# Kernel optimization log

Hardware: AMD Instinct MI355X
Metric: run time of the kernel (lower is better)

Reference implementation:

```python
import jax, jax.numpy as jnp
import numpy as np

N = 100000   # nodes
E = 3200000  # edges per graph
D = 16       # embedding_size, num_heads = 1
ATTN_SLOPE = 0.2   # DGL GATv2Conv negative_slope default
ACT_SLOPE = 0.01   # torch.nn.functional.leaky_relu default (activation arg)


def gatv2_layer(h, src, dst, W_src, b_src, W_dst, b_dst, attn):
    """DGL GATv2Conv with num_heads=1, activation=leaky_relu.
    h: [N, D]; src/dst: [E] int; W_*: [D, D]; b_*: [D]; attn: [D].
    """
    feat_src = h @ W_src + b_src          # [N, D]
    feat_dst = h @ W_dst + b_dst          # [N, D]
    el = feat_src[src]                    # [E, D] gather to edges
    e = jax.nn.leaky_relu(el + feat_dst[dst], ATTN_SLOPE)  # [E, D]
    score = e @ attn                      # [E] attention logits
    # segment softmax over incoming edges of each destination node
    smax = jax.ops.segment_max(score, dst, num_segments=N)
    smax = jnp.where(jnp.isfinite(smax), smax, 0.0)  # empty segments -> 0
    ex = jnp.exp(score - smax[dst])       # [E]
    denom = jax.ops.segment_sum(ex, dst, num_segments=N)  # [N]
    alpha = ex / denom[dst]               # [E]
    rst = jax.ops.segment_sum(alpha[:, None] * el, dst, num_segments=N)  # [N, D]
    return jax.nn.leaky_relu(rst, ACT_SLOPE)


def setup_inputs() -> dict:
    key = jax.random.key(0)
    ks = jax.random.split(key, 16)
    s = 1.0 / np.sqrt(D)
    return {
        "embedding": jax.random.normal(ks[0], (N, D), jnp.float32),
        "src1": jax.random.randint(ks[1], (E,), 0, N, jnp.int32),
        "dst1": jax.random.randint(ks[2], (E,), 0, N, jnp.int32),
        "src2": jax.random.randint(ks[3], (E,), 0, N, jnp.int32),
        "dst2": jax.random.randint(ks[4], (E,), 0, N, jnp.int32),
        "W_src1": jax.random.normal(ks[5], (D, D), jnp.float32) * s,
        "b_src1": jnp.zeros((D,), jnp.float32),
        "W_dst1": jax.random.normal(ks[6], (D, D), jnp.float32) * s,
        "b_dst1": jnp.zeros((D,), jnp.float32),
        "attn1": jax.random.normal(ks[7], (D,), jnp.float32) * s,
        "W_src2": jax.random.normal(ks[8], (D, D), jnp.float32) * s,
        "b_src2": jnp.zeros((D,), jnp.float32),
        "W_dst2": jax.random.normal(ks[9], (D, D), jnp.float32) * s,
        "b_dst2": jnp.zeros((D,), jnp.float32),
        "attn2": jax.random.normal(ks[10], (D,), jnp.float32) * s,
    }


def reference(embedding, src1, dst1, src2, dst2,
              W_src1, b_src1, W_dst1, b_dst1, attn1,
              W_src2, b_src2, W_dst2, b_dst2, attn2):
    user2item = gatv2_layer(embedding, src1, dst1, W_src1, b_src1, W_dst1, b_dst1, attn1)
    item_influence = gatv2_layer(user2item, src2, dst2, W_src2, b_src2, W_dst2, b_dst2, attn2)
    return item_influence  # [N, D]
```

## Files before the change

### kernel.cpp

```cpp
#include <hip/hip_runtime.h>
#include <hip/hip_fp16.h>

#define D 16
#define R 64
#define RBITS 6
#define RMASK 63
#define STRIDE 2560
#define CAP 2560
#define ACCT 512
#define KPT (CAP / ACCT)
#define EPB 8192
#define K1T 1024
#define NB2 1664
#define ATTN_SLOPE 0.2f
#define ACT_SLOPE 0.01f

__device__ __forceinline__ float leaky_a(float v) {
    return v > 0.f ? v : ATTN_SLOPE * v;
}
__device__ __forceinline__ float2 h2f(unsigned u) {
    __half2 h = *(__half2*)&u;
    return __half22float2(h);
}


__device__ void binscatter_tile(int tile, const int* __restrict__ src,
                                const int* __restrict__ dst,
                                int* __restrict__ gcur, unsigned* __restrict__ binned,
                                int E, int NB, char* sb) {
    unsigned* sorted = (unsigned*)sb;
    unsigned short* sposb = (unsigned short*)(sb + 32768);
    int* soffs = (int*)(sb + 49152);
    int* delta = (int*)(sb + 49152 + 4 * NB2);
    int* swsum = (int*)(sb + 49152 + 8 * NB2);
    int tid = threadIdx.x;
    int base = tile * EPB;
    int count = E - base;
    if (count > EPB) count = EPB;
    bool full = (count == EPB);

    for (int i = tid; i < NB; i += K1T) soffs[i] = 0;
    __syncthreads();
    int dd[8];
    if (full) {
        const int4* d4 = (const int4*)(dst + base);
        int4 a = d4[tid], b = d4[K1T + tid];
        dd[0] = a.x; dd[1] = a.y; dd[2] = a.z; dd[3] = a.w;
        dd[4] = b.x; dd[5] = b.y; dd[6] = b.z; dd[7] = b.w;
#pragma unroll
        for (int m = 0; m < 8; m++) atomicAdd(&soffs[dd[m] >> RBITS], 1);
    } else {
        for (int k = 0; k < 8; k++) {
            int e = base + k * K1T + tid;
            if (e < E) atomicAdd(&soffs[dst[e] >> RBITS], 1);
        }
    }
    __syncthreads();
    int i0 = 2 * tid, i1 = 2 * tid + 1;
    int a0 = (i0 < NB) ? soffs[i0] : 0;
    int a1 = (i1 < NB) ? soffs[i1] : 0;
    int pair = a0 + a1;
    int lane = tid & 63, w = tid >> 6;
    int x = pair;
#pragma unroll
    for (int ofs = 1; ofs < 64; ofs <<= 1) {
        int y = __shfl_up(x, ofs, 64);
        if (lane >= ofs) x += y;
    }
    if (lane == 63) swsum[w] = x;
    __syncthreads();
    if (w == 0) {
        int v = (lane < 16) ? swsum[lane] : 0;
        int s = v;
#pragma unroll
        for (int ofs = 1; ofs < 16; ofs <<= 1) {
            int y = __shfl_up(s, ofs, 64);
            if (lane >= ofs) s += y;
        }
        if (lane < 16) swsum[lane] = s - v;
    }
    __syncthreads();
    int excl = x - pair + swsum[w];
    __syncthreads();
    if (i0 < NB) {
        soffs[i0] = excl;
        if (a0 > 0) {
            int res = atomicAdd(&gcur[i0], a0);
            delta[i0] = i0 * STRIDE + res - excl;
        }
    }
    if (i1 < NB) {
        soffs[i1] = excl + a0;
        if (a1 > 0) {
            int res = atomicAdd(&gcur[i1], a1);
            delta[i1] = i1 * STRIDE + res - (excl + a0);
        }
    }
    __syncthreads();
    if (full) {
        const int4* s4 = (const int4*)(src + base);
        int4 sa = s4[tid], sb4 = s4[K1T + tid];
        int ss[8] = {sa.x, sa.y, sa.z, sa.w, sb4.x, sb4.y, sb4.z, sb4.w};
#pragma unroll
        for (int m = 0; m < 8; m++) {
            int b = dd[m] >> RBITS;
            int r = atomicAdd(&soffs[b], 1);
            sorted[r] = ((unsigned)ss[m] << RBITS) | (unsigned)(dd[m] & RMASK);
            sposb[r] = (unsigned short)b;
        }
    } else {
        for (int k = 0; k < 8; k++) {
            int e = base + k * K1T + tid;
            if (e < E) {
                int dv = dst[e];
                int b = dv >> RBITS;
                int r = atomicAdd(&soffs[b], 1);
                sorted[r] = ((unsigned)src[e] << RBITS) | (unsigned)(dv & RMASK);
                sposb[r] = (unsigned short)b;
            }
        }
    }
    __syncthreads();
#pragma unroll
    for (int m = 0; m < 8; m++) {
        int p = m * K1T + tid;
        if (p < count) {
            int b = sposb[p];
            int pos = p + delta[b];
            if (pos < (b + 1) * STRIDE) binned[pos] = sorted[p];
        }
    }
}

__device__ void transform_tile(int tile, const float* __restrict__ h,
                               const float* __restrict__ Ws, const float* __restrict__ bs,
                               const float* __restrict__ Wd, const float* __restrict__ bd,
                               __half* __restrict__ fsh, float* __restrict__ fdst,
                               int N, char* sb) {
    float* sWs = (float*)sb;
    float* sWd = sWs + 256;
    float* sbs = sWd + 256;
    float* sbd = sbs + 16;
    int t = threadIdx.x;
    if (t < 256) { sWs[t] = Ws[t]; sWd[t] = Wd[t]; }
    if (t < 16) { sbs[t] = bs[t]; sbd[t] = bd[t]; }
    __syncthreads();
    int n = tile * K1T + t;
    if (n >= N) return;
    float hv[D];
    const float4* h4 = (const float4*)(h + (size_t)n * D);
#pragma unroll
    for (int k = 0; k < 4; k++) {
        float4 v = h4[k];
        hv[4 * k] = v.x; hv[4 * k + 1] = v.y; hv[4 * k + 2] = v.z; hv[4 * k + 3] = v.w;
    }
    float os[D], od[D];
#pragma unroll
    for (int d = 0; d < D; d++) {
        float ss = sbs[d];
        float sd = sbd[d];
#pragma unroll
        for (int k = 0; k < D; k++) {
            ss += hv[k] * sWs[k * D + d];
            sd += hv[k] * sWd[k * D + d];
        }
        os[d] = ss; od[d] = sd;
    }
    unsigned us[8];
#pragma unroll
    for (int k = 0; k < 8; k++) {
        __half2 hh = __floats2half2_rn(os[2 * k], os[2 * k + 1]);
        us[k] = *(unsigned*)&hh;
    }
    uint4* fo = (uint4*)(fsh + (size_t)n * D);
    fo[0] = make_uint4(us[0], us[1], us[2], us[3]);
    fo[1] = make_uint4(us[4], us[5], us[6], us[7]);
    float4* fd4 = (float4*)(fdst + (size_t)n * D);
#pragma unroll
    for (int k = 0; k < 4; k++)
        fd4[k] = make_float4(od[4 * k], od[4 * k + 1], od[4 * k + 2], od[4 * k + 3]);
}

__global__ void __launch_bounds__(K1T)
k1_kernel(const float* h, const float* Ws, const float* bs,
          const float* Wd, const float* bd,
          __half* fsh, float* fdst,
          const int* srcA, const int* dstA, int* gA, unsigned* binnedA, int EA,
          const int* srcB, const int* dstB, int* gB, unsigned* binnedB, int EB,
          int N, int NB, int B1, int B2, int TT) {
    __shared__ __align__(16) char sb[49152 + 8 * NB2 + 64];
    int bid = blockIdx.x;
    if (bid < B1) {
        binscatter_tile(bid, srcA, dstA, gA, binnedA, EA, NB, sb);
    } else if (bid < B1 + B2) {
        binscatter_tile(bid - B1, srcB, dstB, gB, binnedB, EB, NB, sb);
    } else {
        int t = bid - B1 - B2;
        if (t < TT) transform_tile(t, h, Ws, bs, Wd, bd, fsh, fdst, N, sb);
    }
}


template <bool DO_TAIL>
__global__ void __launch_bounds__(ACCT)
acc_kernel(const unsigned* __restrict__ binned, const int* __restrict__ gcur,
           const __half* __restrict__ fsh, const float* __restrict__ fdst,
           const float* __restrict__ attn, float* __restrict__ out,
           __half* __restrict__ fs2h, float* __restrict__ fd2,
           const float* __restrict__ Ws2, const float* __restrict__ bs2,
           const float* __restrict__ Wd2, const float* __restrict__ bd2,
           int N) {
    __shared__ float sfd[R * D];
    __shared__ int ebuf[CAP];
    __shared__ float exbuf[CAP];
    __shared__ int cstart[R + 1];
    __shared__ int cur[R];
    __shared__ float wtail[544];
    int b = blockIdx.x;
    int tid = threadIdx.x;
    int node0 = b * R;
    int nn = N - node0;
    if (nn > R) nn = R;
    for (int i = tid; i < nn * D; i += ACCT) sfd[i] = fdst[node0 * D + i];
    if (tid <= R) cstart[tid] = 0;
    if (DO_TAIL) {
        if (tid < 256) { wtail[tid] = Ws2[tid]; wtail[256 + tid] = Wd2[tid]; }
        if (tid < 16) { wtail[512 + tid] = bs2[tid]; wtail[528 + tid] = bd2[tid]; }
    }

    float av[D];
#pragma unroll
    for (int k = 0; k < D; k++) av[k] = attn[k];

    int cnt = gcur[b];
    if (cnt > CAP) cnt = CAP;
    int base = b * STRIDE;

    unsigned pls[KPT];
#pragma unroll
    for (int k = 0; k < KPT; k++) {
        int j = k * ACCT + tid;
        pls[k] = (j < cnt) ? binned[base + j] : 0xFFFFFFFFu;
    }
    __syncthreads();

    const uint4* fsh4 = (const uint4*)fsh;
    const uint2* fsq = (const uint2*)fsh;
    const float4* sfd4 = (const float4*)sfd;

#pragma unroll
    for (int k = 0; k < KPT; k++)
        if (pls[k] != 0xFFFFFFFFu) atomicAdd(&cstart[pls[k] & RMASK], 1);

    float exs[KPT];
#pragma unroll
    for (int k = 0; k + 1 < KPT; k += 2) {
        unsigned q0 = pls[k], q1 = pls[k + 1];
        uint4 ua0, ub0, ua1, ub1;
        if (q0 != 0xFFFFFFFFu) {
            int s = q0 >> RBITS;
            ua0 = fsh4[2 * s]; ub0 = fsh4[2 * s + 1];
        }
        if (q1 != 0xFFFFFFFFu) {
            int s = q1 >> RBITS;
            ua1 = fsh4[2 * s]; ub1 = fsh4[2 * s + 1];
        }
        if (q0 != 0xFFFFFFFFu) {
            int loc = q0 & RMASK;
            float4 f0 = sfd4[loc * 4 + 0], f1 = sfd4[loc * 4 + 1];
            float4 f2 = sfd4[loc * 4 + 2], f3 = sfd4[loc * 4 + 3];
            float2 c0 = h2f(ua0.x), c1 = h2f(ua0.y), c2 = h2f(ua0.z), c3 = h2f(ua0.w);
            float2 c4 = h2f(ub0.x), c5 = h2f(ub0.y), c6 = h2f(ub0.z), c7 = h2f(ub0.w);
            float p = leaky_a(c0.x + f0.x) * av[0]  + leaky_a(c0.y + f0.y) * av[1]
                    + leaky_a(c1.x + f0.z) * av[2]  + leaky_a(c1.y + f0.w) * av[3]
                    + leaky_a(c2.x + f1.x) * av[4]  + leaky_a(c2.y + f1.y) * av[5]
                    + leaky_a(c3.x + f1.z) * av[6]  + leaky_a(c3.y + f1.w) * av[7]
                    + leaky_a(c4.x + f2.x) * av[8]  + leaky_a(c4.y + f2.y) * av[9]
                    + leaky_a(c5.x + f2.z) * av[10] + leaky_a(c5.y + f2.w) * av[11]
                    + leaky_a(c6.x + f3.x) * av[12] + leaky_a(c6.y + f3.y) * av[13]
                    + leaky_a(c7.x + f3.z) * av[14] + leaky_a(c7.y + f3.w) * av[15];
            exs[k] = __expf(p);
        }
        if (q1 != 0xFFFFFFFFu) {
            int loc = q1 & RMASK;
            float4 f0 = sfd4[loc * 4 + 0], f1 = sfd4[loc * 4 + 1];
            float4 f2 = sfd4[loc * 4 + 2], f3 = sfd4[loc * 4 + 3];
            float2 c0 = h2f(ua1.x), c1 = h2f(ua1.y), c2 = h2f(ua1.z), c3 = h2f(ua1.w);
            float2 c4 = h2f(ub1.x), c5 = h2f(ub1.y), c6 = h2f(ub1.z), c7 = h2f(ub1.w);
            float p = leaky_a(c0.x + f0.x) * av[0]  + leaky_a(c0.y + f0.y) * av[1]
                    + leaky_a(c1.x + f0.z) * av[2]  + leaky_a(c1.y + f0.w) * av[3]
                    + leaky_a(c2.x + f1.x) * av[4]  + leaky_a(c2.y + f1.y) * av[5]
                    + leaky_a(c3.x + f1.z) * av[6]  + leaky_a(c3.y + f1.w) * av[7]
                    + leaky_a(c4.x + f2.x) * av[8]  + leaky_a(c4.y + f2.y) * av[9]
                    + leaky_a(c5.x + f2.z) * av[10] + leaky_a(c5.y + f2.w) * av[11]
                    + leaky_a(c6.x + f3.x) * av[12] + leaky_a(c6.y + f3.y) * av[13]
                    + leaky_a(c7.x + f3.z) * av[14] + leaky_a(c7.y + f3.w) * av[15];
            exs[k + 1] = __expf(p);
        }
    }
    if (KPT & 1) {
        unsigned q0 = pls[KPT - 1];
        if (q0 != 0xFFFFFFFFu) {
            int s = q0 >> RBITS;
            uint4 ua0 = fsh4[2 * s], ub0 = fsh4[2 * s + 1];
            int loc = q0 & RMASK;
            float4 f0 = sfd4[loc * 4 + 0], f1 = sfd4[loc * 4 + 1];
            float4 f2 = sfd4[loc * 4 + 2], f3 = sfd4[loc * 4 + 3];
            float2 c0 = h2f(ua0.x), c1 = h2f(ua0.y), c2 = h2f(ua0.z), c3 = h2f(ua0.w);
            float2 c4 = h2f(ub0.x), c5 = h2f(ub0.y), c6 = h2f(ub0.z), c7 = h2f(ub0.w);
            float p = leaky_a(c0.x + f0.x) * av[0]  + leaky_a(c0.y + f0.y) * av[1]
                    + leaky_a(c1.x + f0.z) * av[2]  + leaky_a(c1.y + f0.w) * av[3]
                    + leaky_a(c2.x + f1.x) * av[4]  + leaky_a(c2.y + f1.y) * av[5]
                    + leaky_a(c3.x + f1.z) * av[6]  + leaky_a(c3.y + f1.w) * av[7]
                    + leaky_a(c4.x + f2.x) * av[8]  + leaky_a(c4.y + f2.y) * av[9]
                    + leaky_a(c5.x + f2.z) * av[10] + leaky_a(c5.y + f2.w) * av[11]
                    + leaky_a(c6.x + f3.x) * av[12] + leaky_a(c6.y + f3.y) * av[13]
                    + leaky_a(c7.x + f3.z) * av[14] + leaky_a(c7.y + f3.w) * av[15];
            exs[KPT - 1] = __expf(p);
        }
    }
    __syncthreads();
    if (tid < R) {
        int v = cstart[tid];
        int x = v;
#pragma unroll
        for (int ofs = 1; ofs < 64; ofs <<= 1) {
            int y = __shfl_up(x, ofs, 64);
            if (tid >= ofs) x += y;
        }
        cstart[tid] = x - v;
        cur[tid] = x - v;
        if (tid == R - 1) cstart[R] = x;
    }
    __syncthreads();
#pragma unroll
    for (int k = 0; k < KPT; k++) {
        unsigned pl = pls[k];
        if (pl != 0xFFFFFFFFu) {
            int r = atomicAdd(&cur[pl & RMASK], 1);
            ebuf[r] = (int)pl;
            exbuf[r] = exs[k];
        }
    }
    __syncthreads();

    int lane = tid & 63;
    int w = tid >> 6;
    int q = lane & 3;
    int s2 = (lane >> 2) & 3;
    int n2 = lane >> 4;

    float4 acc[2];
    float den[2];
#pragma unroll
    for (int i = 0; i < 2; i++) {
        acc[i] = make_float4(0.f, 0.f, 0.f, 0.f);
        den[i] = 0.f;
    }
#pragma unroll
    for (int i = 0; i < 2; i++) {
        int loc = w * 8 + i * 4 + n2;
        int kb = cstart[loc], ke = cstart[loc + 1];
        int k = kb + s2;
        for (; k + 12 < ke; k += 16) {
            int pl0 = ebuf[k];
            int pl1 = ebuf[k + 4];
            int pl2 = ebuf[k + 8];
            int pl3 = ebuf[k + 12];
            float ex0 = exbuf[k];
            float ex1 = exbuf[k + 4];
            float ex2 = exbuf[k + 8];
            float ex3 = exbuf[k + 12];
            uint2 u0 = fsq[(((unsigned)pl0) >> RBITS) * 4 + q];
            uint2 u1 = fsq[(((unsigned)pl1) >> RBITS) * 4 + q];
            uint2 u2 = fsq[(((unsigned)pl2) >> RBITS) * 4 + q];
            uint2 u3 = fsq[(((unsigned)pl3) >> RBITS) * 4 + q];
            float2 a01 = h2f(u0.x), a23 = h2f(u0.y);
            float2 b01 = h2f(u1.x), b23 = h2f(u1.y);
            float2 c01 = h2f(u2.x), c23 = h2f(u2.y);
            float2 d01 = h2f(u3.x), d23 = h2f(u3.y);
            acc[i].x += ex0 * a01.x + ex1 * b01.x + ex2 * c01.x + ex3 * d01.x;
            acc[i].y += ex0 * a01.y + ex1 * b01.y + ex2 * c01.y + ex3 * d01.y;
            acc[i].z += ex0 * a23.x + ex1 * b23.x + ex2 * c23.x + ex3 * d23.x;
            acc[i].w += ex0 * a23.y + ex1 * b23.y + ex2 * c23.y + ex3 * d23.y;
            den[i] += (ex0 + ex1) + (ex2 + ex3);
        }
        for (; k < ke; k += 4) {
            int pl = ebuf[k];
            float ex = exbuf[k];
            uint2 u = fsq[(((unsigned)pl) >> RBITS) * 4 + q];
            float2 a01 = h2f(u.x), a23 = h2f(u.y);
            acc[i].x += ex * a01.x;
            acc[i].y += ex * a01.y;
            acc[i].z += ex * a23.x;
            acc[i].w += ex * a23.y;
            den[i] += ex;
        }
    }
#pragma unroll
    for (int i = 0; i < 2; i++) {
        float4 a = acc[i];
        float dn = den[i];
#pragma unroll
        for (int m = 4; m <= 8; m <<= 1) {
            a.x += __shfl_xor(a.x, m, 16);
            a.y += __shfl_xor(a.y, m, 16);
            a.z += __shfl_xor(a.z, m, 16);
            a.w += __shfl_xor(a.w, m, 16);
            dn += __shfl_xor(dn, m, 16);
        }
        int loc = w * 8 + i * 4 + n2;
        if (s2 == 0 && loc < nn) {
            float inv = dn > 0.f ? 1.f / dn : 0.f;
            float4 v;
            v.x = a.x * inv; v.x = v.x > 0.f ? v.x : ACT_SLOPE * v.x;
            v.y = a.y * inv; v.y = v.y > 0.f ? v.y : ACT_SLOPE * v.y;
            v.z = a.z * inv; v.z = v.z > 0.f ? v.z : ACT_SLOPE * v.z;
            v.w = a.w * inv; v.w = v.w > 0.f ? v.w : ACT_SLOPE * v.w;
            if (DO_TAIL) {
                *(float4*)&sfd[loc * D + q * 4] = v;
            } else {
                ((float4*)out)[(size_t)(node0 + loc) * 4 + q] = v;
            }
        }
    }
    if (DO_TAIL) {
        __syncthreads();
        int loc = tid >> 2, qq = tid & 3;
        if (tid < 256 && loc < nn) {
            float hvv[16];
#pragma unroll
            for (int k = 0; k < 16; k++) hvv[k] = sfd[loc * D + k];
            float s0 = wtail[512 + 4 * qq], s1 = wtail[513 + 4 * qq];
            float s2v = wtail[514 + 4 * qq], s3 = wtail[515 + 4 * qq];
            float d0 = wtail[528 + 4 * qq], d1 = wtail[529 + 4 * qq];
            float d2v = wtail[530 + 4 * qq], d3 = wtail[531 + 4 * qq];
#pragma unroll
            for (int k = 0; k < 16; k++) {
                float hk = hvv[k];
                const float* wr = &wtail[k * 16 + 4 * qq];
                const float* wr2 = &wtail[256 + k * 16 + 4 * qq];
                s0 += hk * wr[0]; s1 += hk * wr[1]; s2v += hk * wr[2]; s3 += hk * wr[3];
                d0 += hk * wr2[0]; d1 += hk * wr2[1]; d2v += hk * wr2[2]; d3 += hk * wr2[3];
            }
            __half2 p0 = __floats2half2_rn(s0, s1), p1 = __floats2half2_rn(s2v, s3);
            *(uint2*)(fs2h + (size_t)(node0 + loc) * D + 4 * qq) =
                make_uint2(*(unsigned*)&p0, *(unsigned*)&p1);
            *(float4*)(fd2 + (size_t)(node0 + loc) * D + 4 * qq) =
                make_float4(d0, d1, d2v, d3);
        }
    }
}


extern "C" void kernel_launch(void* const* d_in, const int* in_sizes, int n_in,
                              void* d_out, int out_size, void* d_ws, size_t ws_size,
                              hipStream_t stream) {
    const float* emb = (const float*)d_in[0];
    const int* src1 = (const int*)d_in[1];
    const int* dst1 = (const int*)d_in[2];
    const int* src2 = (const int*)d_in[3];
    const int* dst2 = (const int*)d_in[4];
    const float* Wsrc1 = (const float*)d_in[5];
    const float* bsrc1 = (const float*)d_in[6];
    const float* Wdst1 = (const float*)d_in[7];
    const float* bdst1 = (const float*)d_in[8];
    const float* attn1 = (const float*)d_in[9];
    const float* Wsrc2 = (const float*)d_in[10];
    const float* bsrc2 = (const float*)d_in[11];
    const float* Wdst2 = (const float*)d_in[12];
    const float* bdst2 = (const float*)d_in[13];
    const float* attn2 = (const float*)d_in[14];

    const int N = in_sizes[0] / D;
    const int E1 = in_sizes[1];
    const int E2 = in_sizes[3];
    const int NB = (N + R - 1) / R;
    const size_t ndf = (size_t)N * D;

    float* ws = (float*)d_ws;
    float* fd1 = ws;
    float* fd2 = fd1 + ndf;
    __half* fs1h = (__half*)(fd2 + ndf);
    __half* fs2h = fs1h + ndf;
    int* gA = (int*)(fs2h + ndf);
    int* gB = gA + NB2;
    unsigned* binned1 = (unsigned*)(gB + NB2);
    unsigned* binned2big = binned1 + (size_t)NB * STRIDE;
    size_t bigNeed = (size_t)((char*)(binned2big + (size_t)NB * STRIDE) - (char*)d_ws);
    bool big = ws_size >= bigNeed;
    (void)n_in; (void)out_size;

    const int B1 = (E1 + EPB - 1) / EPB;
    const int B2 = (E2 + EPB - 1) / EPB;
    const int TT = (N + K1T - 1) / K1T;

    (void)hipMemsetAsync(gA, 0, 2 * NB2 * sizeof(int), stream);

    if (big) {
        k1_kernel<<<B1 + B2 + TT, K1T, 0, stream>>>(
            emb, Wsrc1, bsrc1, Wdst1, bdst1, fs1h, fd1,
            src1, dst1, gA, binned1, E1,
            src2, dst2, gB, binned2big, E2,
            N, NB, B1, B2, TT);
        acc_kernel<true><<<NB, ACCT, 0, stream>>>(
            binned1, gA, fs1h, fd1, attn1, nullptr,
            fs2h, fd2, Wsrc2, bsrc2, Wdst2, bdst2, N);
        acc_kernel<false><<<NB, ACCT, 0, stream>>>(
            binned2big, gB, fs2h, fd2, attn2, (float*)d_out,
            nullptr, nullptr, nullptr, nullptr, nullptr, nullptr, N);
    } else {
        k1_kernel<<<B1 + TT, K1T, 0, stream>>>(
            emb, Wsrc1, bsrc1, Wdst1, bdst1, fs1h, fd1,
            src1, dst1, gA, binned1, E1,
            src2, dst2, gB, binned1, 0,
            N, NB, B1, 0, TT);
        acc_kernel<true><<<NB, ACCT, 0, stream>>>(
            binned1, gA, fs1h, fd1, attn1, nullptr,
            fs2h, fd2, Wsrc2, bsrc2, Wdst2, bdst2, N);
        k1_kernel<<<B2, K1T, 0, stream>>>(
            emb, Wsrc1, bsrc1, Wdst1, bdst1, fs1h, fd1,
            src2, dst2, gB, binned1, E2,
            src2, dst2, gB, binned1, 0,
            N, NB, B2, 0, 0);
        acc_kernel<false><<<NB, ACCT, 0, stream>>>(
            binned1, gB, fs2h, fd2, attn2, (float*)d_out,
            nullptr, nullptr, nullptr, nullptr, nullptr, nullptr, N);
    }
}
```

Measured before the change: 234.2 us.

## Halve binscatter tile size and pack bin indices to raise k1 occupancy

Halves the edges per block and threads per block in the binning kernel and shrinks the shared-memory scratch to match. This allows more blocks per CU, and launch bounds now request 8. The src loads are hoisted ahead of the histogram and packed into key values early. Bucket indices are packed two per register to cut register pressure. The prefix scan now handles four bins per thread, and one redundant barrier is removed. The trade-offs are twice as many tiles, which means more global atomics on gcur, and less work per block.

```diff
diff --git a/kernel.cpp b/kernel.cpp
--- a/kernel.cpp
+++ b/kernel.cpp
@@ -9,8 +9,8 @@
 #define CAP 2560
 #define ACCT 512
 #define KPT (CAP / ACCT)
-#define EPB 8192
-#define K1T 1024
+#define EPB 4096
+#define K1T 512
 #define NB2 1664
 #define ATTN_SLOPE 0.2f
 #define ACT_SLOPE 0.01f
@@ -29,10 +29,10 @@
                                 int* __restrict__ gcur, unsigned* __restrict__ binned,
                                 int E, int NB, char* sb) {
     unsigned* sorted = (unsigned*)sb;
-    unsigned short* sposb = (unsigned short*)(sb + 32768);
-    int* soffs = (int*)(sb + 49152);
-    int* delta = (int*)(sb + 49152 + 4 * NB2);
-    int* swsum = (int*)(sb + 49152 + 8 * NB2);
+    unsigned short* sposb = (unsigned short*)(sb + 16384);
+    int* soffs = (int*)(sb + 24576);
+    int* delta = (int*)(sb + 24576 + 4 * NB2);
+    int* swsum = (int*)(sb + 24576 + 8 * NB2);
     int tid = threadIdx.x;
     int base = tile * EPB;
     int count = E - base;
@@ -41,14 +41,28 @@
 
     for (int i = tid; i < NB; i += K1T) soffs[i] = 0;
     __syncthreads();
-    int dd[8];
+
+    unsigned val[8];
+    unsigned bp[4];
     if (full) {
         const int4* d4 = (const int4*)(dst + base);
+        const int4* s4 = (const int4*)(src + base);
         int4 a = d4[tid], b = d4[K1T + tid];
-        dd[0] = a.x; dd[1] = a.y; dd[2] = a.z; dd[3] = a.w;
-        dd[4] = b.x; dd[5] = b.y; dd[6] = b.z; dd[7] = b.w;
-#pragma unroll
-        for (int m = 0; m < 8; m++) atomicAdd(&soffs[dd[m] >> RBITS], 1);
+        int4 sa = s4[tid], sb4 = s4[K1T + tid];
+        int dd[8] = {a.x, a.y, a.z, a.w, b.x, b.y, b.z, b.w};
+        int ss[8] = {sa.x, sa.y, sa.z, sa.w, sb4.x, sb4.y, sb4.z, sb4.w};
+#pragma unroll
+        for (int m = 0; m < 8; m++)
+            val[m] = ((unsigned)ss[m] << RBITS) | ((unsigned)dd[m] & RMASK);
+#pragma unroll
+        for (int m = 0; m < 4; m++)
+            bp[m] = ((unsigned)dd[2 * m] >> RBITS) |
+                    (((unsigned)dd[2 * m + 1] >> RBITS) << 16);
+#pragma unroll
+        for (int m = 0; m < 4; m++) {
+            atomicAdd(&soffs[bp[m] & 0xFFFFu], 1);
+            atomicAdd(&soffs[bp[m] >> 16], 1);
+        }
     } else {
         for (int k = 0; k < 8; k++) {
             int e = base + k * K1T + tid;
@@ -56,12 +70,14 @@
         }
     }
     __syncthreads();
-    int i0 = 2 * tid, i1 = 2 * tid + 1;
+    int i0 = 4 * tid;
     int a0 = (i0 < NB) ? soffs[i0] : 0;
-    int a1 = (i1 < NB) ? soffs[i1] : 0;
-    int pair = a0 + a1;
+    int a1 = (i0 + 1 < NB) ? soffs[i0 + 1] : 0;
+    int a2 = (i0 + 2 < NB) ? soffs[i0 + 2] : 0;
+    int a3 = (i0 + 3 < NB) ? soffs[i0 + 3] : 0;
+    int quad = a0 + a1 + a2 + a3;
     int lane = tid & 63, w = tid >> 6;
-    int x = pair;
+    int x = quad;
 #pragma unroll
     for (int ofs = 1; ofs < 64; ofs <<= 1) {
         int y = __shfl_up(x, ofs, 64);
@@ -70,43 +86,46 @@
     if (lane == 63) swsum[w] = x;
     __syncthreads();
     if (w == 0) {
-        int v = (lane < 16) ? swsum[lane] : 0;
+        int v = (lane < 8) ? swsum[lane] : 0;
         int s = v;
 #pragma unroll
-        for (int ofs = 1; ofs < 16; ofs <<= 1) {
+        for (int ofs = 1; ofs < 8; ofs <<= 1) {
             int y = __shfl_up(s, ofs, 64);
             if (lane >= ofs) s += y;
         }
-        if (lane < 16) swsum[lane] = s - v;
-    }
-    __syncthreads();
-    int excl = x - pair + swsum[w];
-    __syncthreads();
+        if (lane < 8) swsum[lane] = s - v;
+    }
+    __syncthreads();
+    int excl = x - quad + swsum[w];
+    int e0 = excl, e1 = excl + a0, e2 = e1 + a1, e3 = e2 + a2;
     if (i0 < NB) {
-        soffs[i0] = excl;
-        if (a0 > 0) {
-            int res = atomicAdd(&gcur[i0], a0);
-            delta[i0] = i0 * STRIDE + res - excl;
-        }
-    }
-    if (i1 < NB) {
-        soffs[i1] = excl + a0;
-        if (a1 > 0) {
-            int res = atomicAdd(&gcur[i1], a1);
-            delta[i1] = i1 * STRIDE + res - (excl + a0);
-        }
+        soffs[i0] = e0;
+        if (a0 > 0) { int res = atomicAdd(&gcur[i0], a0); delta[i0] = i0 * STRIDE + res - e0; }
+    }
+    if (i0 + 1 < NB) {
+        soffs[i0 + 1] = e1;
+        if (a1 > 0) { int res = atomicAdd(&gcur[i0 + 1], a1); delta[i0 + 1] = (i0 + 1) * STRIDE + res - e1; }
+    }
+    if (i0 + 2 < NB) {
+        soffs[i0 + 2] = e2;
+        if (a2 > 0) { int res = atomicAdd(&gcur[i0 + 2], a2); delta[i0 + 2] = (i0 + 2) * STRIDE + res - e2; }
+    }
+    if (i0 + 3 < NB) {
+        soffs[i0 + 3] = e3;
+        if (a3 > 0) { int res = atomicAdd(&gcur[i0 + 3], a3); delta[i0 + 3] = (i0 + 3) * STRIDE + res - e3; }
     }
     __syncthreads();
     if (full) {
-        const int4* s4 = (const int4*)(src + base);
-        int4 sa = s4[tid], sb4 = s4[K1T + tid];
-        int ss[8] = {sa.x, sa.y, sa.z, sa.w, sb4.x, sb4.y, sb4.z, sb4.w};
-#pragma unroll
-        for (int m = 0; m < 8; m++) {
-            int b = dd[m] >> RBITS;
-            int r = atomicAdd(&soffs[b], 1);
-            sorted[r] = ((unsigned)ss[m] << RBITS) | (unsigned)(dd[m] & RMASK);
-            sposb[r] = (unsigned short)b;
+#pragma unroll
+        for (int m = 0; m < 4; m++) {
+            int b0 = bp[m] & 0xFFFFu;
+            int r0 = atomicAdd(&soffs[b0], 1);
+            sorted[r0] = val[2 * m];
+            sposb[r0] = (unsigned short)b0;
+            int b1 = bp[m] >> 16;
+            int r1 = atomicAdd(&soffs[b1], 1);
+            sorted[r1] = val[2 * m + 1];
+            sposb[r1] = (unsigned short)b1;
         }
     } else {
         for (int k = 0; k < 8; k++) {
@@ -181,14 +200,14 @@
         fd4[k] = make_float4(od[4 * k], od[4 * k + 1], od[4 * k + 2], od[4 * k + 3]);
 }
 
-__global__ void __launch_bounds__(K1T)
+__global__ void __launch_bounds__(K1T, 8)
 k1_kernel(const float* h, const float* Ws, const float* bs,
           const float* Wd, const float* bd,
           __half* fsh, float* fdst,
           const int* srcA, const int* dstA, int* gA, unsigned* binnedA, int EA,
           const int* srcB, const int* dstB, int* gB, unsigned* binnedB, int EB,
           int N, int NB, int B1, int B2, int TT) {
-    __shared__ __align__(16) char sb[49152 + 8 * NB2 + 64];
+    __shared__ __align__(16) char sb[24576 + 8 * NB2 + 64];
     int bid = blockIdx.x;
     if (bid < B1) {
         binscatter_tile(bid, srcA, dstA, gA, binnedA, EA, NB, sb);
```

After: 312.8 us. 33.6% more time.

## Double edges per binning tile and reserve global bin slots once per tile

Applied to the files above, without the earlier changes.

Each binning tile now covers 16384 edges, handled as two 8192-edge chunks inside the block. A first histogram pass over the whole tile reserves global bin space with one atomic per bin, and each chunk then writes at running per-bin cursors. This halves the number of global atomics on gcur and the tile count, and makes each bin's writes longer and more contiguous. The cost is reading dst an extra time, more barriers, and half as many blocks to spread across the GPU.

```diff
diff --git a/kernel.cpp b/kernel.cpp
--- a/kernel.cpp
+++ b/kernel.cpp
@@ -9,7 +9,8 @@
 #define CAP 2560
 #define ACCT 512
 #define KPT (CAP / ACCT)
-#define EPB 8192
+#define EPB 16384
+#define CHK 8192
 #define K1T 1024
 #define NB2 1664
 #define ATTN_SLOPE 0.2f
@@ -31,103 +32,152 @@
     unsigned* sorted = (unsigned*)sb;
     unsigned short* sposb = (unsigned short*)(sb + 32768);
     int* soffs = (int*)(sb + 49152);
-    int* delta = (int*)(sb + 49152 + 4 * NB2);
+    int* wcur = (int*)(sb + 49152 + 4 * NB2);
     int* swsum = (int*)(sb + 49152 + 8 * NB2);
     int tid = threadIdx.x;
+    int lane = tid & 63, w = tid >> 6;
     int base = tile * EPB;
     int count = E - base;
     if (count > EPB) count = EPB;
-    bool full = (count == EPB);
-
-    for (int i = tid; i < NB; i += K1T) soffs[i] = 0;
-    __syncthreads();
-    int dd[8];
-    if (full) {
+
+    for (int i = tid; i < NB; i += K1T) wcur[i] = 0;
+    __syncthreads();
+
+    if (count == EPB) {
         const int4* d4 = (const int4*)(dst + base);
-        int4 a = d4[tid], b = d4[K1T + tid];
-        dd[0] = a.x; dd[1] = a.y; dd[2] = a.z; dd[3] = a.w;
-        dd[4] = b.x; dd[5] = b.y; dd[6] = b.z; dd[7] = b.w;
-#pragma unroll
-        for (int m = 0; m < 8; m++) atomicAdd(&soffs[dd[m] >> RBITS], 1);
+#pragma unroll
+        for (int m = 0; m < 4; m++) {
+            int4 a = d4[m * K1T + tid];
+            atomicAdd(&wcur[a.x >> RBITS], 1);
+            atomicAdd(&wcur[a.y >> RBITS], 1);
+            atomicAdd(&wcur[a.z >> RBITS], 1);
+            atomicAdd(&wcur[a.w >> RBITS], 1);
+        }
     } else {
-        for (int k = 0; k < 8; k++) {
+        for (int k = 0; k < 16; k++) {
             int e = base + k * K1T + tid;
-            if (e < E) atomicAdd(&soffs[dst[e] >> RBITS], 1);
-        }
-    }
-    __syncthreads();
+            if (e < E) atomicAdd(&wcur[dst[e] >> RBITS], 1);
+        }
+    }
+    __syncthreads();
+
+    for (int i = tid; i < NB; i += K1T) {
+        int c = wcur[i];
+        if (c > 0) {
+            int res = atomicAdd(&gcur[i], c);
+            wcur[i] = i * STRIDE + res;
+        }
+    }
+    __syncthreads();
+
     int i0 = 2 * tid, i1 = 2 * tid + 1;
-    int a0 = (i0 < NB) ? soffs[i0] : 0;
-    int a1 = (i1 < NB) ? soffs[i1] : 0;
-    int pair = a0 + a1;
-    int lane = tid & 63, w = tid >> 6;
-    int x = pair;
-#pragma unroll
-    for (int ofs = 1; ofs < 64; ofs <<= 1) {
-        int y = __shfl_up(x, ofs, 64);
-        if (lane >= ofs) x += y;
-    }
-    if (lane == 63) swsum[w] = x;
-    __syncthreads();
-    if (w == 0) {
-        int v = (lane < 16) ? swsum[lane] : 0;
-        int s = v;
-#pragma unroll
-        for (int ofs = 1; ofs < 16; ofs <<= 1) {
-            int y = __shfl_up(s, ofs, 64);
-            if (lane >= ofs) s += y;
-        }
-        if (lane < 16) swsum[lane] = s - v;
-    }
-    __syncthreads();
-    int excl = x - pair + swsum[w];
-    __syncthreads();
-    if (i0 < NB) {
-        soffs[i0] = excl;
-        if (a0 > 0) {
-            int res = atomicAdd(&gcur[i0], a0);
-            delta[i0] = i0 * STRIDE + res - excl;
-        }
-    }
-    if (i1 < NB) {
-        soffs[i1] = excl + a0;
-        if (a1 > 0) {
-            int res = atomicAdd(&gcur[i1], a1);
-            delta[i1] = i1 * STRIDE + res - (excl + a0);
-        }
-    }
-    __syncthreads();
-    if (full) {
-        const int4* s4 = (const int4*)(src + base);
-        int4 sa = s4[tid], sb4 = s4[K1T + tid];
-        int ss[8] = {sa.x, sa.y, sa.z, sa.w, sb4.x, sb4.y, sb4.z, sb4.w};
+    for (int c = 0; c < 2; c++) {
+        int cbase = base + c * CHK;
+        int cc = count - c * CHK;
+        if (cc <= 0) break;
+        if (cc > CHK) cc = CHK;
+        bool full = (cc == CHK);
+
+        for (int i = tid; i < NB; i += K1T) soffs[i] = 0;
+        __syncthreads();
+
+        if (full) {
+            const int4* d4 = (const int4*)(dst + cbase);
+            int4 a = d4[tid], b4 = d4[K1T + tid];
+            atomicAdd(&soffs[a.x >> RBITS], 1);
+            atomicAdd(&soffs[a.y >> RBITS], 1);
+            atomicAdd(&soffs[a.z >> RBITS], 1);
+            atomicAdd(&soffs[a.w >> RBITS], 1);
+            atomicAdd(&soffs[b4.x >> RBITS], 1);
+            atomicAdd(&soffs[b4.y >> RBITS], 1);
+            atomicAdd(&soffs[b4.z >> RBITS], 1);
+            atomicAdd(&soffs[b4.w >> RBITS], 1);
+        } else {
+            for (int k = 0; k < 8; k++) {
+                int e = cbase + k * K1T + tid;
+                if (e < E) atomicAdd(&soffs[dst[e] >> RBITS], 1);
+            }
+        }
+        __syncthreads();
+
+        int a0 = (i0 < NB) ? soffs[i0] : 0;
+        int a1 = (i1 < NB) ? soffs[i1] : 0;
+        int pair = a0 + a1;
+        int x = pair;
+#pragma unroll
+        for (int ofs = 1; ofs < 64; ofs <<= 1) {
+            int y = __shfl_up(x, ofs, 64);
+            if (lane >= ofs) x += y;
+        }
+        if (lane == 63) swsum[w] = x;
+        __syncthreads();
+        if (w == 0) {
+            int v = (lane < 16) ? swsum[lane] : 0;
+            int s = v;
+#pragma unroll
+            for (int ofs = 1; ofs < 16; ofs <<= 1) {
+                int y = __shfl_up(s, ofs, 64);
+                if (lane >= ofs) s += y;
+            }
+            if (lane < 16) swsum[lane] = s - v;
+        }
+        __syncthreads();
+        int excl = x - pair + swsum[w];
+        int e0 = excl, e1 = excl + a0;
+        int d0v = 0, d1v = 0;
+        if (i0 < NB) {
+            soffs[i0] = e0;
+            if (a0 > 0) { d0v = wcur[i0] - e0; wcur[i0] = d0v; }
+        }
+        if (i1 < NB) {
+            soffs[i1] = e1;
+            if (a1 > 0) { d1v = wcur[i1] - e1; wcur[i1] = d1v; }
+        }
+        __syncthreads();
+
+        if (full) {
+            const int4* d4 = (const int4*)(dst + cbase);
+            const int4* s4 = (const int4*)(src + cbase);
+            int4 a = d4[tid], b4 = d4[K1T + tid];
+            int4 sa = s4[tid], sb4 = s4[K1T + tid];
+            int dd[8] = {a.x, a.y, a.z, a.w, b4.x, b4.y, b4.z, b4.w};
+            int ss[8] = {sa.x, sa.y, sa.z, sa.w, sb4.x, sb4.y, sb4.z, sb4.w};
+#pragma unroll
+            for (int m = 0; m < 8; m++) {
+                int bb = dd[m] >> RBITS;
+                int r = atomicAdd(&soffs[bb], 1);
+                sorted[r] = ((unsigned)ss[m] << RBITS) | (unsigned)(dd[m] & RMASK);
+                sposb[r] = (unsigned short)bb;
+            }
+        } else {
+            for (int k = 0; k < 8; k++) {
+                int e = cbase + k * K1T + tid;
+                if (e < E) {
+                    int dv = dst[e];
+                    int bb = dv >> RBITS;
+                    int r = atomicAdd(&soffs[bb], 1);
+                    sorted[r] = ((unsigned)src[e] << RBITS) | (unsigned)(dv & RMASK);
+                    sposb[r] = (unsigned short)bb;
+                }
+            }
+        }
+        __syncthreads();
+
 #pragma unroll
         for (int m = 0; m < 8; m++) {
-            int b = dd[m] >> RBITS;
-            int r = atomicAdd(&soffs[b], 1);
-            sorted[r] = ((unsigned)ss[m] << RBITS) | (unsigned)(dd[m] & RMASK);
-            sposb[r] = (unsigned short)b;
-        }
-    } else {
-        for (int k = 0; k < 8; k++) {
-            int e = base + k * K1T + tid;
-            if (e < E) {
-                int dv = dst[e];
-                int b = dv >> RBITS;
-                int r = atomicAdd(&soffs[b], 1);
-                sorted[r] = ((unsigned)src[e] << RBITS) | (unsigned)(dv & RMASK);
-                sposb[r] = (unsigned short)b;
-            }
-        }
-    }
-    __syncthreads();
-#pragma unroll
-    for (int m = 0; m < 8; m++) {
-        int p = m * K1T + tid;
-        if (p < count) {
-            int b = sposb[p];
-            int pos = p + delta[b];
-            if (pos < (b + 1) * STRIDE) binned[pos] = sorted[p];
+            int p = m * K1T + tid;
+            if (p < cc) {
+                int bb = sposb[p];
+                int pos = p + wcur[bb];
+                if (pos < (bb + 1) * STRIDE) binned[pos] = sorted[p];
+            }
+        }
+        __syncthreads();
+
+        if (c == 0) {
+            if (i0 < NB && a0 > 0) wcur[i0] = d0v + e0 + a0;
+            if (i1 < NB && a1 > 0) wcur[i1] = d1v + e1 + a1;
+            __syncthreads();
         }
     }
 }
```

Result: no change. 235.2 us (+0.5%).

## Scatter edges directly to global bins, dropping the shared-memory local sort

Applied to the files above, without the earlier changes.

The binning pass no longer sorts each tile into shared memory with a prefix scan and then copies out. It now counts edges per bin, reserves a global range for each bin with one atomic, and has each thread write its edge straight to the global bin position using shared atomic cursors. The edges per block double while threads per block halve, the transform tile covers 1024 nodes with a loop, and the much smaller shared footprint plus launch bounds of 8 allow higher occupancy. The cost is that global writes are less coalesced, since consecutive threads write to scattered bins instead of sorted runs.

```diff
diff --git a/kernel.cpp b/kernel.cpp
--- a/kernel.cpp
+++ b/kernel.cpp
@@ -9,8 +9,9 @@
 #define CAP 2560
 #define ACCT 512
 #define KPT (CAP / ACCT)
-#define EPB 8192
-#define K1T 1024
+#define EPB 16384
+#define K1T 512
+#define TNODES 1024
 #define NB2 1664
 #define ATTN_SLOPE 0.2f
 #define ACT_SLOPE 0.01f
@@ -28,106 +29,77 @@
                                 const int* __restrict__ dst,
                                 int* __restrict__ gcur, unsigned* __restrict__ binned,
                                 int E, int NB, char* sb) {
-    unsigned* sorted = (unsigned*)sb;
-    unsigned short* sposb = (unsigned short*)(sb + 32768);
-    int* soffs = (int*)(sb + 49152);
-    int* delta = (int*)(sb + 49152 + 4 * NB2);
-    int* swsum = (int*)(sb + 49152 + 8 * NB2);
+    int* wcur = (int*)sb;
     int tid = threadIdx.x;
     int base = tile * EPB;
     int count = E - base;
     if (count > EPB) count = EPB;
-    bool full = (count == EPB);
-
-    for (int i = tid; i < NB; i += K1T) soffs[i] = 0;
-    __syncthreads();
-    int dd[8];
-    if (full) {
+    bool fullT = (count == EPB);
+
+    for (int i = tid; i < NB; i += K1T) wcur[i] = 0;
+    __syncthreads();
+
+    if (fullT) {
         const int4* d4 = (const int4*)(dst + base);
-        int4 a = d4[tid], b = d4[K1T + tid];
-        dd[0] = a.x; dd[1] = a.y; dd[2] = a.z; dd[3] = a.w;
-        dd[4] = b.x; dd[5] = b.y; dd[6] = b.z; dd[7] = b.w;
-#pragma unroll
-        for (int m = 0; m < 8; m++) atomicAdd(&soffs[dd[m] >> RBITS], 1);
+#pragma unroll
+        for (int m = 0; m < EPB / 4 / K1T; m++) {
+            int4 a = d4[m * K1T + tid];
+            atomicAdd(&wcur[a.x >> RBITS], 1);
+            atomicAdd(&wcur[a.y >> RBITS], 1);
+            atomicAdd(&wcur[a.z >> RBITS], 1);
+            atomicAdd(&wcur[a.w >> RBITS], 1);
+        }
     } else {
-        for (int k = 0; k < 8; k++) {
+        for (int k = 0; k < EPB / K1T; k++) {
             int e = base + k * K1T + tid;
-            if (e < E) atomicAdd(&soffs[dst[e] >> RBITS], 1);
-        }
-    }
-    __syncthreads();
-    int i0 = 2 * tid, i1 = 2 * tid + 1;
-    int a0 = (i0 < NB) ? soffs[i0] : 0;
-    int a1 = (i1 < NB) ? soffs[i1] : 0;
-    int pair = a0 + a1;
-    int lane = tid & 63, w = tid >> 6;
-    int x = pair;
-#pragma unroll
-    for (int ofs = 1; ofs < 64; ofs <<= 1) {
-        int y = __shfl_up(x, ofs, 64);
-        if (lane >= ofs) x += y;
-    }
-    if (lane == 63) swsum[w] = x;
-    __syncthreads();
-    if (w == 0) {
-        int v = (lane < 16) ? swsum[lane] : 0;
-        int s = v;
-#pragma unroll
-        for (int ofs = 1; ofs < 16; ofs <<= 1) {
-            int y = __shfl_up(s, ofs, 64);
-            if (lane >= ofs) s += y;
-        }
-        if (lane < 16) swsum[lane] = s - v;
-    }
-    __syncthreads();
-    int excl = x - pair + swsum[w];
-    __syncthreads();
-    if (i0 < NB) {
-        soffs[i0] = excl;
-        if (a0 > 0) {
-            int res = atomicAdd(&gcur[i0], a0);
-            delta[i0] = i0 * STRIDE + res - excl;
-        }
-    }
-    if (i1 < NB) {
-        soffs[i1] = excl + a0;
-        if (a1 > 0) {
-            int res = atomicAdd(&gcur[i1], a1);
-            delta[i1] = i1 * STRIDE + res - (excl + a0);
-        }
-    }
-    __syncthreads();
-    if (full) {
+            if (e < E) atomicAdd(&wcur[dst[e] >> RBITS], 1);
+        }
+    }
+    __syncthreads();
+
+    for (int i = tid; i < NB; i += K1T) {
+        int c = wcur[i];
+        if (c > 0) {
+            int res = atomicAdd(&gcur[i], c);
+            wcur[i] = i * STRIDE + res;
+        }
+    }
+    __syncthreads();
+
+    if (fullT) {
+        const int4* d4 = (const int4*)(dst + base);
         const int4* s4 = (const int4*)(src + base);
-        int4 sa = s4[tid], sb4 = s4[K1T + tid];
-        int ss[8] = {sa.x, sa.y, sa.z, sa.w, sb4.x, sb4.y, sb4.z, sb4.w};
-#pragma unroll
-        for (int m = 0; m < 8; m++) {
-            int b = dd[m] >> RBITS;
-            int r = atomicAdd(&soffs[b], 1);
-            sorted[r] = ((unsigned)ss[m] << RBITS) | (unsigned)(dd[m] & RMASK);
-            sposb[r] = (unsigned short)b;
+#pragma unroll
+        for (int m = 0; m < EPB / 4 / K1T; m++) {
+            int4 a = d4[m * K1T + tid];
+            int4 s = s4[m * K1T + tid];
+            int b0 = a.x >> RBITS;
+            int p0 = atomicAdd(&wcur[b0], 1);
+            if (p0 < (b0 + 1) * STRIDE)
+                binned[p0] = ((unsigned)s.x << RBITS) | (unsigned)(a.x & RMASK);
+            int b1 = a.y >> RBITS;
+            int p1 = atomicAdd(&wcur[b1], 1);
+            if (p1 < (b1 + 1) * STRIDE)
+                binned[p1] = ((unsigned)s.y << RBITS) | (unsigned)(a.y & RMASK);
+            int b2 = a.z >> RBITS;
+            int p2 = atomicAdd(&wcur[b2], 1);
+            if (p2 < (b2 + 1) * STRIDE)
+                binned[p2] = ((unsigned)s.z << RBITS) | (unsigned)(a.z & RMASK);
+            int b3 = a.w >> RBITS;
+            int p3 = atomicAdd(&wcur[b3], 1);
+            if (p3 < (b3 + 1) * STRIDE)
+                binned[p3] = ((unsigned)s.w << RBITS) | (unsigned)(a.w & RMASK);
         }
     } else {
-        for (int k = 0; k < 8; k++) {
+        for (int k = 0; k < EPB / K1T; k++) {
             int e = base + k * K1T + tid;
             if (e < E) {
                 int dv = dst[e];
-                int b = dv >> RBITS;
-                int r = atomicAdd(&soffs[b], 1);
-                sorted[r] = ((unsigned)src[e] << RBITS) | (unsigned)(dv & RMASK);
-                sposb[r] = (unsigned short)b;
+                int bb = dv >> RBITS;
+                int p = atomicAdd(&wcur[bb], 1);
+                if (p < (bb + 1) * STRIDE)
+                    binned[p] = ((unsigned)src[e] << RBITS) | (unsigned)(dv & RMASK);
             }
-        }
-    }
-    __syncthreads();
-#pragma unroll
-    for (int m = 0; m < 8; m++) {
-        int p = m * K1T + tid;
-        if (p < count) {
-            int b = sposb[p];
-            int pos = p + delta[b];
-            if (pos < (b + 1) * STRIDE) binned[pos] = sorted[p];
         }
     }
 }
@@ -145,50 +117,52 @@
     if (t < 256) { sWs[t] = Ws[t]; sWd[t] = Wd[t]; }
     if (t < 16) { sbs[t] = bs[t]; sbd[t] = bd[t]; }
     __syncthreads();
-    int n = tile * K1T + t;
-    if (n >= N) return;
-    float hv[D];
-    const float4* h4 = (const float4*)(h + (size_t)n * D);
-#pragma unroll
-    for (int k = 0; k < 4; k++) {
-        float4 v = h4[k];
-        hv[4 * k] = v.x; hv[4 * k + 1] = v.y; hv[4 * k + 2] = v.z; hv[4 * k + 3] = v.w;
-    }
-    float os[D], od[D];
-#pragma unroll
-    for (int d = 0; d < D; d++) {
-        float ss = sbs[d];
-        float sd = sbd[d];
-#pragma unroll
-        for (int k = 0; k < D; k++) {
-            ss += hv[k] * sWs[k * D + d];
-            sd += hv[k] * sWd[k * D + d];
-        }
-        os[d] = ss; od[d] = sd;
-    }
-    unsigned us[8];
-#pragma unroll
-    for (int k = 0; k < 8; k++) {
-        __half2 hh = __floats2half2_rn(os[2 * k], os[2 * k + 1]);
-        us[k] = *(unsigned*)&hh;
-    }
-    uint4* fo = (uint4*)(fsh + (size_t)n * D);
-    fo[0] = make_uint4(us[0], us[1], us[2], us[3]);
-    fo[1] = make_uint4(us[4], us[5], us[6], us[7]);
-    float4* fd4 = (float4*)(fdst + (size_t)n * D);
-#pragma unroll
-    for (int k = 0; k < 4; k++)
-        fd4[k] = make_float4(od[4 * k], od[4 * k + 1], od[4 * k + 2], od[4 * k + 3]);
-}
-
-__global__ void __launch_bounds__(K1T)
+    for (int kk = 0; kk < TNODES / K1T; kk++) {
+        int n = tile * TNODES + kk * K1T + t;
+        if (n >= N) break;
+        float hv[D];
+        const float4* h4 = (const float4*)(h + (size_t)n * D);
+#pragma unroll
+        for (int k = 0; k < 4; k++) {
+            float4 v = h4[k];
+            hv[4 * k] = v.x; hv[4 * k + 1] = v.y; hv[4 * k + 2] = v.z; hv[4 * k + 3] = v.w;
+        }
+        float os[D], od[D];
+#pragma unroll
+        for (int d = 0; d < D; d++) {
+            float ss = sbs[d];
+            float sd = sbd[d];
+#pragma unroll
+            for (int k = 0; k < D; k++) {
+                ss += hv[k] * sWs[k * D + d];
+                sd += hv[k] * sWd[k * D + d];
+            }
+            os[d] = ss; od[d] = sd;
+        }
+        unsigned us[8];
+#pragma unroll
+        for (int k = 0; k < 8; k++) {
+            __half2 hh = __floats2half2_rn(os[2 * k], os[2 * k + 1]);
+            us[k] = *(unsigned*)&hh;
+        }
+        uint4* fo = (uint4*)(fsh + (size_t)n * D);
+        fo[0] = make_uint4(us[0], us[1], us[2], us[3]);
+        fo[1] = make_uint4(us[4], us[5], us[6], us[7]);
+        float4* fd4 = (float4*)(fdst + (size_t)n * D);
+#pragma unroll
+        for (int k = 0; k < 4; k++)
+            fd4[k] = make_float4(od[4 * k], od[4 * k + 1], od[4 * k + 2], od[4 * k + 3]);
+    }
+}
+
+__global__ void __launch_bounds__(K1T, 8)
 k1_kernel(const float* h, const float* Ws, const float* bs,
           const float* Wd, const float* bd,
           __half* fsh, float* fdst,
           const int* srcA, const int* dstA, int* gA, unsigned* binnedA, int EA,
           const int* srcB, const int* dstB, int* gB, unsigned* binnedB, int EB,
           int N, int NB, int B1, int B2, int TT) {
-    __shared__ __align__(16) char sb[49152 + 8 * NB2 + 64];
+    __shared__ __align__(16) char sb[4 * NB2 + 64];
     int bid = blockIdx.x;
     if (bid < B1) {
         binscatter_tile(bid, srcA, dstA, gA, binnedA, EA, NB, sb);
@@ -493,7 +467,7 @@
 
     const int B1 = (E1 + EPB - 1) / EPB;
     const int B2 = (E2 + EPB - 1) / EPB;
-    const int TT = (N + K1T - 1) / K1T;
+    const int TT = (N + TNODES - 1) / TNODES;
 
     (void)hipMemsetAsync(gA, 0, 2 * NB2 * sizeof(int), stream);
 
```

New measurement: 416.1 us. 1.78x slower.
